# Kernel tuning notes

Hardware: AMD Instinct MI355X
Metric: run time of the kernel (lower is better)

Reference implementation:

```python
import jax, jax.numpy as jnp
import numpy as np

FEATURES_DIM = 64 * (64 * 10 + 1)  # 41024
BASE = 64 * 10 + 1                 # 641
B = 1024


def encode_boards(boards):
    """Vectorized HalfKP encode. boards: [B,8,8] int in 0..12.
    0 = my king, 12 = opp king, 6 = empty, 1..5 my pieces, 7..11 opp pieces.
    Returns [B, 2*FEATURES_DIM] float32 = concat(opps, mys) per original code."""
    nb = boards.shape[0]
    d = boards.reshape(nb, 64)
    sq = jnp.arange(64, dtype=jnp.int32)
    my_king = jnp.argmax(d == 0, axis=1).astype(jnp.int32)    # [B]
    opp_king = jnp.argmax(d == 12, axis=1).astype(jnp.int32)  # [B]
    is_my = (d >= 1) & (d <= 5)
    is_opp = (d >= 7) & (d <= 11)
    # MY_PIECE_TYPES index = piece-1 ; OPP_PIECE_TYPES [11,10,9,8,7] index = 11-piece
    my_idx = my_king[:, None] * BASE + (d - 1) * 64 + sq
    opp_idx = opp_king[:, None] * BASE + (11 - d) * 64 + sq
    my_idx = jnp.where(is_my, my_idx, FEATURES_DIM)    # out-of-range -> dropped
    opp_idx = jnp.where(is_opp, opp_idx, FEATURES_DIM)
    rows = jnp.arange(nb)[:, None]
    mys = jnp.zeros((nb, FEATURES_DIM), jnp.float32).at[rows, my_idx].set(1.0, mode='drop')
    opps = jnp.zeros((nb, FEATURES_DIM), jnp.float32).at[rows, opp_idx].set(1.0, mode='drop')
    return jnp.concatenate([opps, mys], axis=1)


def setup_inputs() -> dict:
    key = jax.random.key(0)
    ks = jax.random.split(key, 12)
    # boards: values 1..11 everywhere, then place exactly one my-king (0) and one opp-king (12)
    bf = jax.random.randint(ks[0], (B, 64), 1, 12, dtype=jnp.int32)
    mk = jax.random.randint(ks[1], (B,), 0, 32)
    ok = jax.random.randint(ks[2], (B,), 32, 64)
    rows = jnp.arange(B)
    bf = bf.at[rows, mk].set(0).at[rows, ok].set(12)
    boards = bf.reshape(B, 8, 8)
    s = 0.02
    W_my = jax.random.normal(ks[3], (256, FEATURES_DIM), jnp.float32) * s
    b_my = jax.random.normal(ks[4], (256,), jnp.float32) * s
    W_opp = jax.random.normal(ks[5], (256, FEATURES_DIM), jnp.float32) * s
    b_opp = jax.random.normal(ks[6], (256,), jnp.float32) * s
    W1 = jax.random.normal(ks[7], (32, 512), jnp.float32) * s
    b1 = jnp.zeros((32,), jnp.float32)
    W2 = jax.random.normal(ks[8], (32, 32), jnp.float32) * s
    b2 = jnp.zeros((32,), jnp.float32)
    W3 = jax.random.normal(ks[9], (1, 32), jnp.float32) * s
    b3 = jnp.zeros((1,), jnp.float32)
    return {"boards": boards, "W_my": W_my, "b_my": b_my, "W_opp": W_opp,
            "b_opp": b_opp, "W1": W1, "b1": b1, "W2": W2, "b2": b2,
            "W3": W3, "b3": b3}


def reference(boards, W_my, b_my, W_opp, b_opp, W1, b1, W2, b2, W3, b3):
    feats = encode_boards(boards)              # [B, 2*FEATURES_DIM] = (opps, mys)
    # NOTE: faithful to original: my_pieces consumes the FIRST half (which is opps)
    my_in = feats[:, :FEATURES_DIM]
    opp_in = feats[:, FEATURES_DIM:]
    my_pos = jax.nn.relu(my_in @ W_my.T + b_my)     # [B,256]
    opp_pos = jax.nn.relu(opp_in @ W_opp.T + b_opp) # [B,256]
    h = jnp.concatenate([my_pos, opp_pos], axis=1)  # [B,512]
    h = jax.nn.relu(h @ W1.T + b1)
    h = jax.nn.relu(h @ W2.T + b2)
    out = h @ W3.T + b3                             # [B,1]
    return out.reshape(-1)
```

## Files before the change

kernel.cpp:

```cpp
#include <hip/hip_runtime.h>

#define FD     41024
#define KBASE  641
#define WIN    320
#define NB_MAX 1024
#define BCAP   96

#define WS_OFF0  0
#define WS_OFF1  (NB_MAX*64)
#define WS_N0    (2*NB_MAX*64)
#define WS_N1    (WS_N0 + NB_MAX)
#define WS_KMY   (WS_N1 + NB_MAX)
#define WS_KOPP  (WS_KMY + NB_MAX)
#define WS_BCNT  (WS_KOPP + NB_MAX)
#define WS_BUCK  (WS_BCNT + 128)
#define WS_H     (WS_BUCK + 2*64*BCAP)

__global__ __launch_bounds__(64) void classify(
    const int* __restrict__ boards, int* __restrict__ ws)
{
    __shared__ int s_off0[64], s_off1[64];
    __shared__ int s_cnt[2], s_k[2];
    const int b = blockIdx.x;
    const int t = threadIdx.x;

    s_off0[t] = 0; s_off1[t] = 0;
    if (t < 2) s_cnt[t] = 0;
    __syncthreads();

    const int d = boards[b * 64 + t];
    if (d == 0)       s_k[0] = t;
    else if (d == 12) s_k[1] = t;
    else if (d >= 1 && d <= 5) { int p = atomicAdd(&s_cnt[1], 1); s_off1[p] = (d - 1) * 64 + t; }
    else if (d >= 7 && d <= 11){ int p = atomicAdd(&s_cnt[0], 1); s_off0[p] = (11 - d) * 64 + t; }
    __syncthreads();

    ws[WS_OFF0 + b * 64 + t] = s_off0[t];
    ws[WS_OFF1 + b * 64 + t] = s_off1[t];
    if (t == 0) {
        ws[WS_N0   + b] = s_cnt[0];
        ws[WS_N1   + b] = s_cnt[1];
        ws[WS_KMY  + b] = s_k[0];
        ws[WS_KOPP + b] = s_k[1];
        int i0 = atomicAdd(&ws[WS_BCNT + 0 * 64 + s_k[1]], 1);
        if (i0 < BCAP) ws[WS_BUCK + (0 * 64 + s_k[1]) * BCAP + i0] = b;
        int i1 = atomicAdd(&ws[WS_BCNT + 1 * 64 + s_k[0]], 1);
        if (i1 < BCAP) ws[WS_BUCK + (1 * 64 + s_k[0]) * BCAP + i1] = b;
    }
}

__global__ __launch_bounds__(256) void gather_bucketed(
    const float* __restrict__ W_my, const float* __restrict__ W_opp,
    const float* __restrict__ b_my, const float* __restrict__ b_opp,
    const int* __restrict__ ws, float* __restrict__ h)
{
    __shared__ float win[WIN * 33];
    __shared__ int   goffs[8 * 64];
    __shared__ int   s_list[BCAP];
    __shared__ int   s_nb;

    const int blk = blockIdx.x;
    const int rg  = blk & 7;
    const int k   = (blk >> 3) & 63;
    const int m   = blk >> 9;
    const int t   = threadIdx.x;

    if (t == 0) s_nb = ws[WS_BCNT + m * 64 + k];
    __syncthreads();
    int n_b = s_nb;
    if (n_b == 0) return;
    if (n_b > BCAP) n_b = BCAP;

    if (t < n_b) s_list[t] = ws[WS_BUCK + (m * 64 + k) * BCAP + t];

    const float* __restrict__ W = m ? W_opp : W_my;
    const size_t gbase = (size_t)(rg * 32) * FD + (size_t)k * KBASE;
    #pragma unroll
    for (int u = 0; u < 40; u++) {
        const int idx = u * 256 + t;
        const int r = idx / WIN;
        const int c = idx - r * WIN;
        win[c * 33 + r] = W[gbase + (size_t)r * FD + c];
    }
    __syncthreads();

    const int* __restrict__ offarr = ws + (m ? WS_OFF1 : WS_OFF0);
    const int* __restrict__ narr   = ws + (m ? WS_N1   : WS_N0);
    const float bias = (m ? b_opp : b_my)[rg * 32 + (t & 31)];
    const int r    = t & 31;
    const int slot = t >> 5;
    const int hcol = m * 256 + rg * 32 + r;

    for (int g = 0; g < n_b; g += 8) {
        #pragma unroll
        for (int u = 0; u < 2; u++) {
            const int j  = u * 256 + t;
            const int bi = g + (j >> 6);
            if (bi < n_b) goffs[j] = offarr[s_list[bi] * 64 + (j & 63)];
        }
        __syncthreads();

        const int bi = g + slot;
        if (bi < n_b) {
            const int board = s_list[bi];
            const int nf = narr[board];
            const int* __restrict__ lo = &goffs[slot * 64];
            float acc0 = 0.0f, acc1 = 0.0f;
            int i = 0;
            for (; i + 4 <= nf; i += 4) {
                acc0 += win[lo[i]     * 33 + r] + win[lo[i + 1] * 33 + r];
                acc1 += win[lo[i + 2] * 33 + r] + win[lo[i + 3] * 33 + r];
            }
            for (; i < nf; i++) acc0 += win[lo[i] * 33 + r];
            h[(size_t)board * 512 + hcol] = fmaxf(acc0 + acc1 + bias, 0.0f);
        }
        __syncthreads();
    }
}

__global__ __launch_bounds__(256) void mlp_tail(
    const float* __restrict__ h,
    const float* __restrict__ W1, const float* __restrict__ b1,
    const float* __restrict__ W2, const float* __restrict__ b2,
    const float* __restrict__ W3, const float* __restrict__ b3,
    float* __restrict__ out)
{
    __shared__ float s_h[512];
    __shared__ float s_h1[32];
    const int b = blockIdx.x;
    const int t = threadIdx.x;

    s_h[t]       = h[(size_t)b * 512 + t];
    s_h[256 + t] = h[(size_t)b * 512 + 256 + t];
    __syncthreads();

    {
        const int o = t >> 3, l = t & 7;
        const float* __restrict__ w = W1 + o * 512;
        float p = 0.0f;
        for (int kk = l; kk < 512; kk += 8) p += s_h[kk] * w[kk];
        p += __shfl_down(p, 4, 8);
        p += __shfl_down(p, 2, 8);
        p += __shfl_down(p, 1, 8);
        if (l == 0) s_h1[o] = fmaxf(p + b1[o], 0.0f);
    }
    __syncthreads();

    if (t < 32) {
        const float* __restrict__ w = W2 + t * 32;
        float acc = b2[t];
        for (int kk = 0; kk < 32; kk++) acc += s_h1[kk] * w[kk];
        float h2 = fmaxf(acc, 0.0f);
        float p = h2 * W3[t];
        p += __shfl_down(p, 16, 32);
        p += __shfl_down(p,  8, 32);
        p += __shfl_down(p,  4, 32);
        p += __shfl_down(p,  2, 32);
        p += __shfl_down(p,  1, 32);
        if (t == 0) out[b] = p + b3[0];
    }
}

__global__ __launch_bounds__(256) void nnue_fwd(
    const int*   __restrict__ boards,
    const float* __restrict__ W_my,  const float* __restrict__ b_my,
    const float* __restrict__ W_opp, const float* __restrict__ b_opp,
    const float* __restrict__ W1,    const float* __restrict__ b1,
    const float* __restrict__ W2,    const float* __restrict__ b2,
    const float* __restrict__ W3,    const float* __restrict__ b3,
    float* __restrict__ out)
{
    __shared__ int   s_off0[64], s_off1[64];
    __shared__ int   s_cnt[2], s_kings[2];
    __shared__ float s_h[512];
    __shared__ float s_h1[32];

    const int b = blockIdx.x;
    const int t = threadIdx.x;

    if (t < 2) s_cnt[t] = 0;
    __syncthreads();

    if (t < 64) {
        int d = boards[b * 64 + t];
        if (d == 0)       s_kings[0] = t;
        else if (d == 12) s_kings[1] = t;
        else if (d >= 1 && d <= 5) { int p = atomicAdd(&s_cnt[1], 1); s_off1[p] = (d - 1) * 64 + t; }
        else if (d >= 7)           { int p = atomicAdd(&s_cnt[0], 1); s_off0[p] = (11 - d) * 64 + t; }
    }
    __syncthreads();

    const int n0 = s_cnt[0], n1 = s_cnt[1];
    const int base0 = s_kings[1] * KBASE;
    const int base1 = s_kings[0] * KBASE;

    {
        const float* __restrict__ w = W_my + (size_t)t * FD + base0;
        float acc = b_my[t];
        for (int i = 0; i < n0; i++) acc += w[s_off0[i]];
        s_h[t] = fmaxf(acc, 0.0f);
    }
    {
        const float* __restrict__ w = W_opp + (size_t)t * FD + base1;
        float acc = b_opp[t];
        for (int i = 0; i < n1; i++) acc += w[s_off1[i]];
        s_h[256 + t] = fmaxf(acc, 0.0f);
    }
    __syncthreads();

    {
        const int o = t >> 3, l = t & 7;
        const float* __restrict__ w = W1 + o * 512;
        float p = 0.0f;
        for (int kk = l; kk < 512; kk += 8) p += s_h[kk] * w[kk];
        p += __shfl_down(p, 4, 8);
        p += __shfl_down(p, 2, 8);
        p += __shfl_down(p, 1, 8);
        if (l == 0) s_h1[o] = fmaxf(p + b1[o], 0.0f);
    }
    __syncthreads();

    if (t < 32) {
        const float* __restrict__ w = W2 + t * 32;
        float acc = b2[t];
        for (int kk = 0; kk < 32; kk++) acc += s_h1[kk] * w[kk];
        float h2 = fmaxf(acc, 0.0f);
        float p = h2 * W3[t];
        p += __shfl_down(p, 16, 32);
        p += __shfl_down(p,  8, 32);
        p += __shfl_down(p,  4, 32);
        p += __shfl_down(p,  2, 32);
        p += __shfl_down(p,  1, 32);
        if (t == 0) out[b] = p + b3[0];
    }
}

extern "C" void kernel_launch(void* const* d_in, const int* in_sizes, int n_in,
                              void* d_out, int out_size, void* d_ws, size_t ws_size,
                              hipStream_t stream) {
    const int*   boards = (const int*)  d_in[0];
    const float* W_my   = (const float*)d_in[1];
    const float* b_my   = (const float*)d_in[2];
    const float* W_opp  = (const float*)d_in[3];
    const float* b_opp  = (const float*)d_in[4];
    const float* W1     = (const float*)d_in[5];
    const float* b1     = (const float*)d_in[6];
    const float* W2     = (const float*)d_in[7];
    const float* b2     = (const float*)d_in[8];
    const float* W3     = (const float*)d_in[9];
    const float* b3     = (const float*)d_in[10];
    float* out = (float*)d_out;

    const int nb = in_sizes[0] / 64;
    const size_t ws_needed = (size_t)(WS_H + (size_t)NB_MAX * 512) * sizeof(int);

    if (nb <= NB_MAX && ws_size >= ws_needed) {
        int*   wsi = (int*)d_ws;
        float* h   = (float*)d_ws + WS_H;
        hipMemsetAsync((char*)d_ws + (size_t)WS_BCNT * sizeof(int), 0,
                       128 * sizeof(int), stream);
        classify<<<nb, 64, 0, stream>>>(boards, wsi);
        gather_bucketed<<<1024, 256, 0, stream>>>(W_my, W_opp, b_my, b_opp, wsi, h);
        mlp_tail<<<nb, 256, 0, stream>>>(h, W1, b1, W2, b2, W3, b3, out);
    } else {
        nnue_fwd<<<nb, 256, 0, stream>>>(boards, W_my, b_my, W_opp, b_opp,
                                         W1, b1, W2, b2, W3, b3, out);
    }
}
```

Baseline: 150.8 us.

## Fuse MLP tail into gather via last-arriver counters and drop bucket atomics

Replaces the global atomic bucket lists with a per-block scan of king positions to build each block's board list, which removes the memset and the BCAP cap. The MLP tail is fused into the gather kernel: each block increments a per-board arrival counter, and the 16th contributor runs the 512→32→32→1 MLP for that board. This removes a kernel launch and the separate pass over h, at the cost of every block scanning all board kings, device-scope atomics and fences, and a serialized tail loop in whichever blocks finish last.

```diff
diff --git a/kernel.cpp b/kernel.cpp
--- a/kernel.cpp
+++ b/kernel.cpp
@@ -4,7 +4,6 @@
 #define KBASE  641
 #define WIN    320
 #define NB_MAX 1024
-#define BCAP   96
 
 #define WS_OFF0  0
 #define WS_OFF1  (NB_MAX*64)
@@ -12,9 +11,8 @@
 #define WS_N1    (WS_N0 + NB_MAX)
 #define WS_KMY   (WS_N1 + NB_MAX)
 #define WS_KOPP  (WS_KMY + NB_MAX)
-#define WS_BCNT  (WS_KOPP + NB_MAX)
-#define WS_BUCK  (WS_BCNT + 128)
-#define WS_H     (WS_BUCK + 2*64*BCAP)
+#define WS_FLAG  (WS_KOPP + NB_MAX)
+#define WS_H     (WS_FLAG + NB_MAX)
 
 __global__ __launch_bounds__(64) void classify(
     const int* __restrict__ boards, int* __restrict__ ws)
@@ -42,22 +40,27 @@
         ws[WS_N1   + b] = s_cnt[1];
         ws[WS_KMY  + b] = s_k[0];
         ws[WS_KOPP + b] = s_k[1];
-        int i0 = atomicAdd(&ws[WS_BCNT + 0 * 64 + s_k[1]], 1);
-        if (i0 < BCAP) ws[WS_BUCK + (0 * 64 + s_k[1]) * BCAP + i0] = b;
-        int i1 = atomicAdd(&ws[WS_BCNT + 1 * 64 + s_k[0]], 1);
-        if (i1 < BCAP) ws[WS_BUCK + (1 * 64 + s_k[0]) * BCAP + i1] = b;
-    }
-}
-
-__global__ __launch_bounds__(256) void gather_bucketed(
+        ws[WS_FLAG + b] = 0;
+    }
+}
+
+__global__ __launch_bounds__(256) void gather_tail(
     const float* __restrict__ W_my, const float* __restrict__ W_opp,
     const float* __restrict__ b_my, const float* __restrict__ b_opp,
-    const int* __restrict__ ws, float* __restrict__ h)
+    const float* __restrict__ W1,   const float* __restrict__ b1,
+    const float* __restrict__ W2,   const float* __restrict__ b2,
+    const float* __restrict__ W3,   const float* __restrict__ b3,
+    int* __restrict__ ws, float* __restrict__ h, int* __restrict__ flag,
+    float* __restrict__ out, int nb)
 {
     __shared__ float win[WIN * 33];
     __shared__ int   goffs[8 * 64];
-    __shared__ int   s_list[BCAP];
-    __shared__ int   s_nb;
+    __shared__ int   s_list[NB_MAX];
+    __shared__ int   s_cnt;
+    __shared__ int   s_win[256];
+    __shared__ int   s_wcnt;
+    __shared__ float s_h[512];
+    __shared__ float s_h1[32];
 
     const int blk = blockIdx.x;
     const int rg  = blk & 7;
@@ -65,13 +68,16 @@
     const int m   = blk >> 9;
     const int t   = threadIdx.x;
 
-    if (t == 0) s_nb = ws[WS_BCNT + m * 64 + k];
-    __syncthreads();
-    int n_b = s_nb;
+    if (t == 0) s_cnt = 0;
+    __syncthreads();
+
+    const int* __restrict__ karr = ws + (m ? WS_KMY : WS_KOPP);
+    for (int i = t; i < nb; i += 256)
+        if (karr[i] == k) { int p = atomicAdd(&s_cnt, 1); s_list[p] = i; }
+    __syncthreads();
+
+    const int n_b = s_cnt;
     if (n_b == 0) return;
-    if (n_b > BCAP) n_b = BCAP;
-
-    if (t < n_b) s_list[t] = ws[WS_BUCK + (m * 64 + k) * BCAP + t];
 
     const float* __restrict__ W = m ? W_opp : W_my;
     const size_t gbase = (size_t)(rg * 32) * FD + (size_t)k * KBASE;
@@ -116,48 +122,55 @@
         }
         __syncthreads();
     }
-}
-
-__global__ __launch_bounds__(256) void mlp_tail(
-    const float* __restrict__ h,
-    const float* __restrict__ W1, const float* __restrict__ b1,
-    const float* __restrict__ W2, const float* __restrict__ b2,
-    const float* __restrict__ W3, const float* __restrict__ b3,
-    float* __restrict__ out)
-{
-    __shared__ float s_h[512];
-    __shared__ float s_h1[32];
-    const int b = blockIdx.x;
-    const int t = threadIdx.x;
-
-    s_h[t]       = h[(size_t)b * 512 + t];
-    s_h[256 + t] = h[(size_t)b * 512 + 256 + t];
-    __syncthreads();
-
-    {
-        const int o = t >> 3, l = t & 7;
-        const float* __restrict__ w = W1 + o * 512;
-        float p = 0.0f;
-        for (int kk = l; kk < 512; kk += 8) p += s_h[kk] * w[kk];
-        p += __shfl_down(p, 4, 8);
-        p += __shfl_down(p, 2, 8);
-        p += __shfl_down(p, 1, 8);
-        if (l == 0) s_h1[o] = fmaxf(p + b1[o], 0.0f);
-    }
-    __syncthreads();
-
-    if (t < 32) {
-        const float* __restrict__ w = W2 + t * 32;
-        float acc = b2[t];
-        for (int kk = 0; kk < 32; kk++) acc += s_h1[kk] * w[kk];
-        float h2 = fmaxf(acc, 0.0f);
-        float p = h2 * W3[t];
-        p += __shfl_down(p, 16, 32);
-        p += __shfl_down(p,  8, 32);
-        p += __shfl_down(p,  4, 32);
-        p += __shfl_down(p,  2, 32);
-        p += __shfl_down(p,  1, 32);
-        if (t == 0) out[b] = p + b3[0];
+
+    __syncthreads();
+    __threadfence();
+
+    for (int base = 0; base < n_b; base += 256) {
+        int old = -1, board = -1;
+        const int i = base + t;
+        if (i < n_b) {
+            board = s_list[i];
+            old = __hip_atomic_fetch_add(&flag[board], 1,
+                                         __ATOMIC_ACQ_REL, __HIP_MEMORY_SCOPE_AGENT);
+        }
+        if (t == 0) s_wcnt = 0;
+        __syncthreads();
+        if (old == 15) { int p = atomicAdd(&s_wcnt, 1); s_win[p] = board; }
+        __syncthreads();
+
+        const int nw = s_wcnt;
+        for (int wi = 0; wi < nw; wi++) {
+            const int wb = s_win[wi];
+            s_h[t]       = h[(size_t)wb * 512 + t];
+            s_h[256 + t] = h[(size_t)wb * 512 + 256 + t];
+            __syncthreads();
+            {
+                const int o = t >> 3, l = t & 7;
+                const float* __restrict__ w = W1 + o * 512;
+                float p = 0.0f;
+                for (int kk = l; kk < 512; kk += 8) p += s_h[kk] * w[kk];
+                p += __shfl_down(p, 4, 8);
+                p += __shfl_down(p, 2, 8);
+                p += __shfl_down(p, 1, 8);
+                if (l == 0) s_h1[o] = fmaxf(p + b1[o], 0.0f);
+            }
+            __syncthreads();
+            if (t < 32) {
+                const float* __restrict__ w = W2 + t * 32;
+                float acc = b2[t];
+                for (int kk = 0; kk < 32; kk++) acc += s_h1[kk] * w[kk];
+                float h2 = fmaxf(acc, 0.0f);
+                float p = h2 * W3[t];
+                p += __shfl_down(p, 16, 32);
+                p += __shfl_down(p,  8, 32);
+                p += __shfl_down(p,  4, 32);
+                p += __shfl_down(p,  2, 32);
+                p += __shfl_down(p,  1, 32);
+                if (t == 0) out[wb] = p + b3[0];
+            }
+            __syncthreads();
+        }
     }
 }
 
@@ -255,13 +268,13 @@
     const size_t ws_needed = (size_t)(WS_H + (size_t)NB_MAX * 512) * sizeof(int);
 
     if (nb <= NB_MAX && ws_size >= ws_needed) {
-        int*   wsi = (int*)d_ws;
-        float* h   = (float*)d_ws + WS_H;
-        hipMemsetAsync((char*)d_ws + (size_t)WS_BCNT * sizeof(int), 0,
-                       128 * sizeof(int), stream);
+        int*   wsi  = (int*)d_ws;
+        int*   flag = wsi + WS_FLAG;
+        float* h    = (float*)d_ws + WS_H;
         classify<<<nb, 64, 0, stream>>>(boards, wsi);
-        gather_bucketed<<<1024, 256, 0, stream>>>(W_my, W_opp, b_my, b_opp, wsi, h);
-        mlp_tail<<<nb, 256, 0, stream>>>(h, W1, b1, W2, b2, W3, b3, out);
+        gather_tail<<<1024, 256, 0, stream>>>(W_my, W_opp, b_my, b_opp,
+                                              W1, b1, W2, b2, W3, b3,
+                                              wsi, h, flag, out, nb);
     } else {
         nnue_fwd<<<nb, 256, 0, stream>>>(boards, W_my, b_my, W_opp, b_opp,
                                          W1, b1, W2, b2, W3, b3, out);
```

Result: slower. 406.3 us (+169.3%).

## Build king buckets in-block, drop memset, vectorize weight window loads

Applied to the files above, without the earlier changes.

Removes the global bucket arrays, their atomics and the memset. Each gather block now scans all boards' king indices and builds its own board list in shared memory. The weight window is loaded with aligned float4 reads into a row-major LDS layout (row stride 324), and offsets are fetched as int4. This removes a memset launch and the scalar strided loads, at the cost of every block scanning up to 1024 king entries, some LDS bank conflicts in the row-major layout, and a larger LDS footprint.

```diff
diff --git a/kernel.cpp b/kernel.cpp
--- a/kernel.cpp
+++ b/kernel.cpp
@@ -3,8 +3,8 @@
 #define FD     41024
 #define KBASE  641
 #define WIN    320
+#define SLDS   324
 #define NB_MAX 1024
-#define BCAP   96
 
 #define WS_OFF0  0
 #define WS_OFF1  (NB_MAX*64)
@@ -12,9 +12,7 @@
 #define WS_N1    (WS_N0 + NB_MAX)
 #define WS_KMY   (WS_N1 + NB_MAX)
 #define WS_KOPP  (WS_KMY + NB_MAX)
-#define WS_BCNT  (WS_KOPP + NB_MAX)
-#define WS_BUCK  (WS_BCNT + 128)
-#define WS_H     (WS_BUCK + 2*64*BCAP)
+#define WS_H     (WS_KOPP + NB_MAX)
 
 __global__ __launch_bounds__(64) void classify(
     const int* __restrict__ boards, int* __restrict__ ws)
@@ -42,22 +40,18 @@
         ws[WS_N1   + b] = s_cnt[1];
         ws[WS_KMY  + b] = s_k[0];
         ws[WS_KOPP + b] = s_k[1];
-        int i0 = atomicAdd(&ws[WS_BCNT + 0 * 64 + s_k[1]], 1);
-        if (i0 < BCAP) ws[WS_BUCK + (0 * 64 + s_k[1]) * BCAP + i0] = b;
-        int i1 = atomicAdd(&ws[WS_BCNT + 1 * 64 + s_k[0]], 1);
-        if (i1 < BCAP) ws[WS_BUCK + (1 * 64 + s_k[0]) * BCAP + i1] = b;
     }
 }
 
 __global__ __launch_bounds__(256) void gather_bucketed(
     const float* __restrict__ W_my, const float* __restrict__ W_opp,
     const float* __restrict__ b_my, const float* __restrict__ b_opp,
-    const int* __restrict__ ws, float* __restrict__ h)
-{
-    __shared__ float win[WIN * 33];
+    const int* __restrict__ ws, float* __restrict__ h, int nb)
+{
+    __shared__ float win[32 * SLDS];
+    __shared__ int   s_list[NB_MAX];
     __shared__ int   goffs[8 * 64];
-    __shared__ int   s_list[BCAP];
-    __shared__ int   s_nb;
+    __shared__ int   s_cnt;
 
     const int blk = blockIdx.x;
     const int rg  = blk & 7;
@@ -65,38 +59,51 @@
     const int m   = blk >> 9;
     const int t   = threadIdx.x;
 
-    if (t == 0) s_nb = ws[WS_BCNT + m * 64 + k];
-    __syncthreads();
-    int n_b = s_nb;
+    if (t == 0) s_cnt = 0;
+    __syncthreads();
+
+    const int* __restrict__ karr = ws + (m ? WS_KMY : WS_KOPP);
+    for (int i = t; i < nb; i += 256)
+        if (karr[i] == k) { int p = atomicAdd(&s_cnt, 1); s_list[p] = i; }
+    __syncthreads();
+
+    const int n_b = s_cnt;
     if (n_b == 0) return;
-    if (n_b > BCAP) n_b = BCAP;
-
-    if (t < n_b) s_list[t] = ws[WS_BUCK + (m * 64 + k) * BCAP + t];
-
+
+    const int shift = (k * KBASE) & 3;
+    const int cs    = k * KBASE - shift;
     const float* __restrict__ W = m ? W_opp : W_my;
-    const size_t gbase = (size_t)(rg * 32) * FD + (size_t)k * KBASE;
+    const size_t gbase = (size_t)(rg * 32) * FD + (size_t)cs;
     #pragma unroll
-    for (int u = 0; u < 40; u++) {
+    for (int u = 0; u < 11; u++) {
         const int idx = u * 256 + t;
-        const int r = idx / WIN;
-        const int c = idx - r * WIN;
-        win[c * 33 + r] = W[gbase + (size_t)r * FD + c];
+        if (idx < 2592) {
+            const int r  = idx / 81;
+            const int c4 = idx - r * 81;
+            const float4 v = *(const float4*)(W + gbase + (size_t)r * FD + c4 * 4);
+            *(float4*)(&win[r * SLDS + c4 * 4]) = v;
+        }
     }
     __syncthreads();
 
     const int* __restrict__ offarr = ws + (m ? WS_OFF1 : WS_OFF0);
     const int* __restrict__ narr   = ws + (m ? WS_N1   : WS_N0);
-    const float bias = (m ? b_opp : b_my)[rg * 32 + (t & 31)];
     const int r    = t & 31;
     const int slot = t >> 5;
+    const float bias = (m ? b_opp : b_my)[rg * 32 + r];
     const int hcol = m * 256 + rg * 32 + r;
+    const float* __restrict__ wrow = &win[r * SLDS + shift];
 
     for (int g = 0; g < n_b; g += 8) {
-        #pragma unroll
-        for (int u = 0; u < 2; u++) {
-            const int j  = u * 256 + t;
-            const int bi = g + (j >> 6);
-            if (bi < n_b) goffs[j] = offarr[s_list[bi] * 64 + (j & 63)];
+        {
+            const int j  = t;
+            if (j < 128) {
+                const int bi = g + (j >> 4);
+                if (bi < n_b) {
+                    const int4 v = *(const int4*)(offarr + s_list[bi] * 64 + (j & 15) * 4);
+                    *(int4*)(&goffs[j * 4]) = v;
+                }
+            }
         }
         __syncthreads();
 
@@ -108,10 +115,10 @@
             float acc0 = 0.0f, acc1 = 0.0f;
             int i = 0;
             for (; i + 4 <= nf; i += 4) {
-                acc0 += win[lo[i]     * 33 + r] + win[lo[i + 1] * 33 + r];
-                acc1 += win[lo[i + 2] * 33 + r] + win[lo[i + 3] * 33 + r];
+                acc0 += wrow[lo[i]]     + wrow[lo[i + 1]];
+                acc1 += wrow[lo[i + 2]] + wrow[lo[i + 3]];
             }
-            for (; i < nf; i++) acc0 += win[lo[i] * 33 + r];
+            for (; i < nf; i++) acc0 += wrow[lo[i]];
             h[(size_t)board * 512 + hcol] = fmaxf(acc0 + acc1 + bias, 0.0f);
         }
         __syncthreads();
@@ -257,10 +264,8 @@
     if (nb <= NB_MAX && ws_size >= ws_needed) {
         int*   wsi = (int*)d_ws;
         float* h   = (float*)d_ws + WS_H;
-        hipMemsetAsync((char*)d_ws + (size_t)WS_BCNT * sizeof(int), 0,
-                       128 * sizeof(int), stream);
         classify<<<nb, 64, 0, stream>>>(boards, wsi);
-        gather_bucketed<<<1024, 256, 0, stream>>>(W_my, W_opp, b_my, b_opp, wsi, h);
+        gather_bucketed<<<1024, 256, 0, stream>>>(W_my, W_opp, b_my, b_opp, wsi, h, nb);
         mlp_tail<<<nb, 256, 0, stream>>>(h, W1, b1, W2, b2, W3, b3, out);
     } else {
         nnue_fwd<<<nb, 256, 0, stream>>>(boards, W_my, b_my, W_opp, b_opp,
```

After: 145.5 us (median of 2 runs). 1.04x faster.
